# Optimization experiments

Measured on AMD Instinct MI355X. Metric: run time of the kernel, lower is better.

The kernel has to match this reference:

```python
import jax, jax.numpy as jnp
import numpy as np


def setup_inputs() -> dict:
    key = jax.random.key(0)
    ks = jax.random.split(key, 7)
    t, e, h = 2048, 512, 8
    s = 0.02
    return {
        "x": jax.random.normal(ks[0], (t, e), jnp.float32),
        "y": jax.random.normal(ks[1], (t, e), jnp.float32),
        "Wk": jax.random.normal(ks[2], (e, e * h), jnp.float32) * s,
        "Wq": jax.random.normal(ks[3], (e, e * h), jnp.float32) * s,
        "Wv": jax.random.normal(ks[4], (e, e * h), jnp.float32) * s,
        "Wu": jax.random.normal(ks[5], (e * h, e), jnp.float32) * s,
        "bu": jnp.zeros((e,), jnp.float32),
    }


def reference(x, y, Wk, Wq, Wv, Wu, bu):
    t, e = x.shape
    h = Wk.shape[1] // e
    scale = e ** (-0.25)
    # projections -> [h, t, e] (head dim equals emb in this 'wide' attention)
    k = (x @ Wk).reshape(t, h, e).transpose(1, 0, 2) * scale
    q = (y @ Wq).reshape(t, h, e).transpose(1, 0, 2) * scale
    v = (x @ Wv).reshape(t, h, e).transpose(1, 0, 2)
    # scores [h, t, t]
    dot = jnp.einsum('hte,hse->hts', q, k)
    attn = jax.nn.softmax(dot, axis=-1)
    out = jnp.einsum('hts,hse->hte', attn, v)          # [h, t, e]
    out = out.transpose(1, 0, 2).reshape(t, h * e)     # [t, h*e]
    return (out @ Wu + bu)[None]                       # [1, t, e] (b=1 in original)
```

## Files before the change

### kernel.cpp

```cpp
#include <hip/hip_runtime.h>
#include <hip/hip_bf16.h>
#include <stdint.h>

#define T_SEQ 2048
#define EMB   512
#define NH    8
#define HEAD_ALL 4096

typedef __attribute__((ext_vector_type(8))) short short8;
typedef __attribute__((ext_vector_type(4))) float f32x4;

__device__ __forceinline__ unsigned short f2b(float f) {
    __hip_bfloat16 h = __float2bfloat16(f);
    return *reinterpret_cast<unsigned short*>(&h);
}
__device__ __forceinline__ float b2f(unsigned short u) {
    return __uint_as_float(((unsigned)u) << 16);
}
__device__ __forceinline__ void gload_lds16(const void* g, void* l) {
    __builtin_amdgcn_global_load_lds((__attribute__((address_space(1))) void*)(void*)(g),
                                     (__attribute__((address_space(3))) void*)(l), 16, 0, 0);
}
__device__ __forceinline__ void wg_barrier() {
    asm volatile("" ::: "memory");
    __builtin_amdgcn_s_barrier();
    asm volatile("" ::: "memory");
}

__global__ void cvt_bf16_2(const float* __restrict__ a, const float* __restrict__ b,
                           unsigned short* __restrict__ oa, unsigned short* __restrict__ ob, int n8) {
    const float* in = blockIdx.y ? b : a;
    unsigned short* out = blockIdx.y ? ob : oa;
    int i = blockIdx.x * 256 + threadIdx.x;
    if (i >= n8) return;
    const f32x4* p = (const f32x4*)in + 2 * (size_t)i;
    f32x4 va = p[0], vb = p[1];
    uint4 o;
    o.x = (unsigned)f2b(va[0]) | ((unsigned)f2b(va[1]) << 16);
    o.y = (unsigned)f2b(va[2]) | ((unsigned)f2b(va[3]) << 16);
    o.z = (unsigned)f2b(vb[0]) | ((unsigned)f2b(vb[1]) << 16);
    o.w = (unsigned)f2b(vb[2]) | ((unsigned)f2b(vb[3]) << 16);
    *((uint4*)out + i) = o;
}

__global__ void transpose_cvt3_f32(const float* __restrict__ w0, const float* __restrict__ w1,
                                   const float* __restrict__ w2, unsigned short* __restrict__ out,
                                   int R, int C, long outS) {
    __shared__ unsigned short t[64][66];
    const int z = blockIdx.z;
    const float* in = (z == 0) ? w0 : ((z == 1) ? w1 : w2);
    unsigned short* ob = out + (long)z * outS;
    const int tid = threadIdx.x;
    const int r0 = blockIdx.y * 64, c0 = blockIdx.x * 64;
#pragma unroll
    for (int it = 0; it < 4; ++it) {
        int flat = it * 256 + tid;
        int r = flat >> 4, c4 = flat & 15;
        f32x4 v = *(const f32x4*)(in + (long)(r0 + r) * C + c0 + c4 * 4);
#pragma unroll
        for (int w = 0; w < 4; ++w) t[r][c4 * 4 + w] = f2b(v[w]);
    }
    __syncthreads();
#pragma unroll
    for (int it = 0; it < 2; ++it) {
        int flat = it * 256 + tid;
        int rr = flat >> 3, c8 = flat & 7;
        unsigned u[4];
#pragma unroll
        for (int w = 0; w < 4; ++w) {
            unsigned short a = t[c8 * 8 + 2 * w][rr];
            unsigned short b = t[c8 * 8 + 2 * w + 1][rr];
            u[w] = (unsigned)a | ((unsigned)b << 16);
        }
        *(uint4*)(ob + (long)(c0 + rr) * R + r0 + c8 * 8) = make_uint4(u[0], u[1], u[2], u[3]);
    }
}

__global__ void transpose_bf16(const unsigned short* __restrict__ in, unsigned short* __restrict__ out,
                               int R, int C, long inS, long outS) {
    __shared__ unsigned short t[64][66];
    const unsigned short* ib = in + (long)blockIdx.z * inS;
    unsigned short* ob = out + (long)blockIdx.z * outS;
    const int tid = threadIdx.x;
    const int r0 = blockIdx.y * 64, c0 = blockIdx.x * 64;
#pragma unroll
    for (int it = 0; it < 2; ++it) {
        int flat = it * 256 + tid;
        int r = flat >> 3, c8 = flat & 7;
        uint4 v = *(const uint4*)(ib + (long)(r0 + r) * C + c0 + c8 * 8);
        unsigned u[4] = {v.x, v.y, v.z, v.w};
#pragma unroll
        for (int w = 0; w < 4; ++w) {
            t[r][c8 * 8 + 2 * w]     = (unsigned short)(u[w] & 0xffff);
            t[r][c8 * 8 + 2 * w + 1] = (unsigned short)(u[w] >> 16);
        }
    }
    __syncthreads();
#pragma unroll
    for (int it = 0; it < 2; ++it) {
        int flat = it * 256 + tid;
        int rr = flat >> 3, c8 = flat & 7;
        unsigned u[4];
#pragma unroll
        for (int w = 0; w < 4; ++w)
            u[w] = (unsigned)t[c8 * 8 + 2 * w][rr] | ((unsigned)t[c8 * 8 + 2 * w + 1][rr] << 16);
        *(uint4*)(ob + (long)(c0 + rr) * R + r0 + c8 * 8) = make_uint4(u[0], u[1], u[2], u[3]);
    }
}

template<int R_>
__device__ __forceinline__ void stage2(const unsigned short* __restrict__ src, int kfull,
                                       short* ldsbase, int i, int tid, int wid) {
#pragma unroll
    for (int s = 0; s < 2; ++s) {
        const int ii = i + s;
        const int r = ii * 64 + (tid >> 3);
        const int d = (tid & 7) * 16;
        const int sc = (d ^ ((r & 7) << 4)) >> 1;
        gload_lds16(src + (long)r * kfull + sc, ldsbase + ii * 4096 + wid * 512);
    }
}

template<int BM, int BN, int KTILES, int MODE>
__global__ __launch_bounds__(512, 2)
void gemm8p(const unsigned short* __restrict__ A, const unsigned short* __restrict__ A2,
            const unsigned short* __restrict__ B, void* __restrict__ Cout,
            int kfull, float alpha, long As, long Bs, long Cs, int ldc)
{
    static_assert(KTILES >= 3, "pipeline needs >=3 K-tiles");
    constexpr int ATILE = BM * 64;
    constexpr int BTILE = BN * 64;
    constexpr int LA = BM / 64;
    constexpr int LB = BN / 64;
    constexpr int MF = BM / 32;
    constexpr int NF = BN / 64;
    constexpr int MFP = MF / 4;

    __shared__ __align__(16) short lds[2 * (ATILE + BTILE)];

    const int tid = threadIdx.x;
    const int wid = tid >> 6, lane = tid & 63;
    const int wm = wid >> 2, wn = wid & 3;
    const int fr = lane & 15, fq = lane >> 4;

    const int nwg = gridDim.x * gridDim.y * gridDim.z;
    int flat = blockIdx.x + gridDim.x * (blockIdx.y + gridDim.y * blockIdx.z);
    flat = (flat & 7) * (nwg >> 3) + (flat >> 3);
    const int bx = flat % gridDim.x;
    const int rem = flat / gridDim.x;
    const int by = rem % gridDim.y;
    const long batch = rem / gridDim.y;

    const int bm = by * BM, bn = bx * BN;

    const unsigned short* Ab;
    const unsigned short* Bb;
    int koff = 0;
    if constexpr (MODE == 1) { Ab = (batch == 2) ? A2 : A; Bb = B + batch * Bs; }
    else { Ab = A; Bb = B; koff = (int)batch * (KTILES * 64); }

    const unsigned short* Ag = Ab + (long)bm * kfull + koff;
    const unsigned short* Bg = Bb + (long)bn * kfull + koff;

    f32x4 acc[MF][NF];
#pragma unroll
    for (int i = 0; i < MF; i++)
#pragma unroll
        for (int j = 0; j < NF; j++) acc[i][j] = 0.f;

#pragma unroll
    for (int i = 0; i < LA; i += 2) stage2<BM>(Ag, kfull, lds, i, tid, wid);
#pragma unroll
    for (int i = 0; i < LB; i += 2) stage2<BN>(Bg, kfull, lds + 2 * ATILE, i, tid, wid);
#pragma unroll
    for (int i = 0; i < LB; i += 2) stage2<BN>(Bg + 64, kfull, lds + 2 * ATILE + BTILE, i, tid, wid);
    if constexpr (LB == 4) asm volatile("s_waitcnt vmcnt(4)" ::: "memory");
    else                   asm volatile("s_waitcnt vmcnt(2)" ::: "memory");
    wg_barrier();

#pragma unroll 2
    for (int t = 0; t < KTILES; ++t) {
        short* la  = lds + (t & 1) * ATILE;
        short* laN = lds + ((t + 1) & 1) * ATILE;
        short* lb  = lds + 2 * ATILE + (t & 1) * BTILE;
        const int kA = (t + 1) * 64;
        const int kB = (t + 2) * 64;

        short8 bfrag[NF][2];
#pragma unroll
        for (int q = 0; q < 4; ++q) {
            if (q == 0) {
#pragma unroll
                for (int nf = 0; nf < NF; ++nf)
#pragma unroll
                    for (int kk = 0; kk < 2; ++kk) {
                        const int r = wn * (BN / 4) + nf * 16 + fr;
                        const int cb = kk * 64 + fq * 16;
                        bfrag[nf][kk] = *(const short8*)(lb + r * 64 + ((cb ^ ((r & 7) << 4)) >> 1));
                    }
            }
            short8 afrag[MFP][2];
#pragma unroll
            for (int mf = 0; mf < MFP; ++mf)
#pragma unroll
                for (int kk = 0; kk < 2; ++kk) {
                    const int r = wm * (BM / 2) + q * (BM / 8) + mf * 16 + fr;
                    const int cb = kk * 64 + fq * 16;
                    afrag[mf][kk] = *(const short8*)(la + r * 64 + ((cb ^ ((r & 7) << 4)) >> 1));
                }
            if (t + 1 < KTILES) {
                if (q == 0) stage2<BM>(Ag + kA, kfull, laN, 0, tid, wid);
                if (q == 1 && LA == 4) stage2<BM>(Ag + kA, kfull, laN, 2, tid, wid);
            }
            if (t + 2 < KTILES) {
                if (q == 2) stage2<BN>(Bg + kB, kfull, lb, 0, tid, wid);
                if (q == 3 && LB == 4) stage2<BN>(Bg + kB, kfull, lb, 2, tid, wid);
            }
            wg_barrier();
            __builtin_amdgcn_s_setprio(1);
#pragma unroll
            for (int mf = 0; mf < MFP; ++mf)
#pragma unroll
                for (int nf = 0; nf < NF; ++nf)
#pragma unroll
                    for (int kk = 0; kk < 2; ++kk)
                        acc[q * MFP + mf][nf] = __builtin_amdgcn_mfma_f32_16x16x32_bf16(
                            afrag[mf][kk], bfrag[nf][kk], acc[q * MFP + mf][nf], 0, 0, 0);
            __builtin_amdgcn_s_setprio(0);
            if (q == 3) {
                if (t + 2 < KTILES) {
                    if constexpr (LB == 4) asm volatile("s_waitcnt vmcnt(4)" ::: "memory");
                    else                   asm volatile("s_waitcnt vmcnt(2)" ::: "memory");
                } else {
                    asm volatile("s_waitcnt vmcnt(0)" ::: "memory");
                }
            }
            wg_barrier();
        }
    }

#pragma unroll
    for (int m = 0; m < MF; ++m)
#pragma unroll
        for (int j = 0; j < 4; ++j) {
            const int row = bm + wm * (BM / 2) + m * 16 + fq * 4 + j;
#pragma unroll
            for (int n = 0; n < NF; ++n) {
                const int col = bn + wn * (BN / 4) + n * 16 + fr;
                const float v = acc[m][n][j] * alpha;
                if constexpr (MODE == 1) {
                    unsigned short* C = (unsigned short*)Cout + batch * Cs;
                    C[(long)(col >> 9) * ((long)T_SEQ * EMB) + (long)row * EMB + (col & 511)] = f2b(v);
                } else {
                    float* C = (float*)Cout + batch * ((long)T_SEQ * EMB);
                    C[(long)row * ldc + col] = v;
                }
            }
        }
}

__global__ __launch_bounds__(512, 1)
void attn_fused(const unsigned short* __restrict__ Qg, const unsigned short* __restrict__ Kg,
                const unsigned short* __restrict__ VTg, unsigned short* __restrict__ Og,
                float scale)
{
    __shared__ __align__(16) short lds[69888];
    float* rs = (float*)(lds + 69632);
    char* ldsb = (char*)lds;

    const int tid = threadIdx.x;
    const int wid = tid >> 6, lane = tid & 63;
    const int fr = lane & 15, fq = lane >> 4;
    const int rg = wid >> 1, ch = wid & 1;

    const int orig = blockIdx.x + 32 * blockIdx.y;
    const int f = (orig & 7) * 32 + (orig >> 3);
    const int qb = f & 31, h = f >> 5;
    const long TE = (long)T_SEQ * EMB;
    const unsigned short* Qh = Qg + (long)h * TE + (long)(qb * 64) * EMB;
    const unsigned short* Kh = Kg + (long)h * TE;
    const unsigned short* Vh = VTg + (long)h * TE;

    short8 qreg[16];
#pragma unroll
    for (int ks = 0; ks < 16; ++ks)
        qreg[ks] = *(const short8*)(Qh + (long)(rg * 16 + fr) * EMB + ks * 32 + fq * 8);

    auto stageK = [&](int kb) {
#pragma unroll
        for (int it = 0; it < 8; ++it) {
            const int c = it * 512 + tid;
            const int kv = c >> 6, s = c & 63;
            gload_lds16(Kh + (long)(kb * 64 + kv) * EMB + (((s * 16) ^ ((kv & 7) << 4)) >> 1),
                        lds + (it * 512 + wid * 64) * 8);
        }
    };
    auto stageV = [&](int kb) {
#pragma unroll
        for (int it = 0; it < 8; ++it) {
            const int c = it * 512 + tid;
            const int d = c >> 3, s = c & 7;
            gload_lds16(Vh + (long)d * T_SEQ + kb * 64 + (((s * 16) ^ ((d & 7) << 4)) >> 1),
                        lds + 32768 + (it * 512 + wid * 64) * 8);
        }
    };

    f32x4 oacc[4][4];
#pragma unroll
    for (int m = 0; m < 4; ++m)
#pragma unroll
        for (int n = 0; n < 4; ++n) oacc[m][n] = 0.f;
    float rsum[4] = {0.f, 0.f, 0.f, 0.f};

    stageK(0);
    stageV(0);

#pragma unroll 1
    for (int t = 0; t < 32; ++t) {
        asm volatile("s_waitcnt vmcnt(8)" ::: "memory");
        wg_barrier();

        f32x4 sacc[2][2];
#pragma unroll
        for (int c = 0; c < 2; ++c) { sacc[c][0] = 0.f; sacc[c][1] = 0.f; }
#pragma unroll
        for (int ks = 0; ks < 16; ++ks) {
#pragma unroll
            for (int c = 0; c < 2; ++c) {
                const int kv = (ch * 2 + c) * 16 + fr;
                const short8 bfr = *(const short8*)(ldsb + kv * 1024 +
                                    ((ks * 64 + fq * 16) ^ ((kv & 7) << 4)));
                sacc[c][ks & 1] = __builtin_amdgcn_mfma_f32_16x16x32_bf16(
                    qreg[ks], bfr, sacc[c][ks & 1], 0, 0, 0);
            }
        }
#pragma unroll
        for (int c = 0; c < 2; ++c)
#pragma unroll
            for (int j = 0; j < 4; ++j) {
                const float v = __expf(scale * (sacc[c][0][j] + sacc[c][1][j]));
                rsum[j] += v;
                const int row = rg * 16 + fq * 4 + j;
                const int kv = (ch * 2 + c) * 16 + fr;
                *(unsigned short*)(ldsb + 131072 + row * 128 +
                    ((kv * 2) ^ ((row & 7) << 4) ^ ((row & 8) << 2))) = f2b(v);
            }
        asm volatile("s_waitcnt lgkmcnt(0)" ::: "memory");
        asm volatile("s_waitcnt vmcnt(0)" ::: "memory");
        wg_barrier();
        if (t + 1 < 32) stageK(t + 1);

#pragma unroll
        for (int kk = 0; kk < 2; ++kk) {
            short8 sa[4], vb[4];
#pragma unroll
            for (int m = 0; m < 4; ++m) {
                const int row = m * 16 + fr;
                sa[m] = *(const short8*)(ldsb + 131072 + row * 128 +
                          ((kk * 64 + fq * 16) ^ ((row & 7) << 4) ^ ((row & 8) << 2)));
            }
#pragma unroll
            for (int n = 0; n < 4; ++n) {
                const int d = wid * 64 + n * 16 + fr;
                vb[n] = *(const short8*)(ldsb + 65536 + d * 128 +
                          ((kk * 64 + fq * 16) ^ ((d & 7) << 4)));
            }
            __builtin_amdgcn_s_setprio(1);
#pragma unroll
            for (int m = 0; m < 4; ++m)
#pragma unroll
                for (int n = 0; n < 4; ++n)
                    oacc[m][n] = __builtin_amdgcn_mfma_f32_16x16x32_bf16(
                        sa[m], vb[n], oacc[m][n], 0, 0, 0);
            __builtin_amdgcn_s_setprio(0);
        }
        wg_barrier();
        if (t + 1 < 32) stageV(t + 1);
    }

#pragma unroll
    for (int j = 0; j < 4; ++j) {
        float v = rsum[j];
        v += __shfl_xor(v, 1);
        v += __shfl_xor(v, 2);
        v += __shfl_xor(v, 4);
        v += __shfl_xor(v, 8);
        if (fr == 0) rs[ch * 64 + rg * 16 + fq * 4 + j] = v;
    }
    asm volatile("s_waitcnt lgkmcnt(0)" ::: "memory");
    wg_barrier();

#pragma unroll
    for (int m = 0; m < 4; ++m)
#pragma unroll
        for (int j = 0; j < 4; ++j) {
            const int row = m * 16 + fq * 4 + j;
            const float rinv = 1.0f / (rs[row] + rs[64 + row]);
#pragma unroll
            for (int n = 0; n < 4; ++n) {
                const int d = wid * 64 + n * 16 + fr;
                Og[(long)(qb * 64 + row) * HEAD_ALL + h * EMB + d] = f2b(oacc[m][n][j] * rinv);
            }
        }
}

__global__ void reduce_bias(const float* __restrict__ part, const float* __restrict__ bias,
                            float* __restrict__ out) {
    const int i = blockIdx.x * 256 + threadIdx.x;
    const long stride4 = (long)T_SEQ * EMB / 4;
    const f32x4* p = (const f32x4*)part;
    f32x4 s = p[i];
#pragma unroll
    for (int sl = 1; sl < 8; ++sl) s += p[i + sl * stride4];
    f32x4 b = *(const f32x4*)(bias + ((i * 4) % EMB));
    *((f32x4*)out + i) = s + b;
}

extern "C" void kernel_launch(void* const* d_in, const int* in_sizes, int n_in,
                              void* d_out, int out_size, void* d_ws, size_t ws_size,
                              hipStream_t stream)
{
    const float* x  = (const float*)d_in[0];
    const float* y  = (const float*)d_in[1];
    const float* Wk = (const float*)d_in[2];
    const float* Wq = (const float*)d_in[3];
    const float* Wv = (const float*)d_in[4];
    const float* Wu = (const float*)d_in[5];
    const float* bu = (const float*)d_in[6];
    char* ws = (char*)d_ws;
    const size_t MB = 1024ull * 1024ull;

    unsigned short* xb   = (unsigned short*)(ws + 0);
    unsigned short* yb   = (unsigned short*)(ws + 2 * MB);
    unsigned short* WT3  = (unsigned short*)(ws + 4 * MB);
    unsigned short* PRJ  = (unsigned short*)(ws + 48 * MB);
    unsigned short* Vb   = (unsigned short*)(ws + 48 * MB);
    unsigned short* Kb   = (unsigned short*)(ws + 64 * MB);
    unsigned short* Qb   = (unsigned short*)(ws + 80 * MB);
    unsigned short* WuT  = (unsigned short*)(ws + 96 * MB);
    unsigned short* VTb  = (unsigned short*)(ws + 100 * MB);
    unsigned short* Ob   = (unsigned short*)(ws + 116 * MB);
    float*          part = (float*)(ws + 0);

    const float scale2 = 0.04419417382415922f;
    const long TE = (long)T_SEQ * EMB;

    cvt_bf16_2<<<dim3(512, 2), dim3(256), 0, stream>>>(x, y, xb, yb, T_SEQ * EMB / 8);
    transpose_cvt3_f32<<<dim3(HEAD_ALL / 64, EMB / 64, 3), dim3(256), 0, stream>>>(
        Wv, Wk, Wq, WT3, EMB, HEAD_ALL, (long)2 * MB);
    transpose_cvt3_f32<<<dim3(EMB / 64, HEAD_ALL / 64, 1), dim3(256), 0, stream>>>(
        Wu, nullptr, nullptr, WuT, HEAD_ALL, EMB, 0);

    gemm8p<256, 256, 8, 1><<<dim3(HEAD_ALL / 256, T_SEQ / 256, 3), 512, 0, stream>>>(
        xb, yb, WT3, PRJ, EMB, 1.f, 0, (long)2 * MB, (long)8 * MB, 0);

    transpose_bf16<<<dim3(EMB / 64, T_SEQ / 64, NH), dim3(256), 0, stream>>>(
        Vb, VTb, T_SEQ, EMB, TE, TE);

    attn_fused<<<dim3(32, 8), 512, 0, stream>>>(Qb, Kb, VTb, Ob, scale2);

    gemm8p<256, 128, 8, 3><<<dim3(EMB / 128, T_SEQ / 256, 8), 512, 0, stream>>>(
        Ob, nullptr, WuT, part, HEAD_ALL, 1.f, 0, 0, 0, EMB);

    reduce_bias<<<dim3(T_SEQ * EMB / 4 / 256), dim3(256), 0, stream>>>(part, bu, (float*)d_out);
}
```

Before: 181.1 us.

## Software-pipeline attention: double-buffer 32-key K/V tiles and overlap QK with PV

Shrinks the key block from 64 to 32 and double-buffers the K, V and probability tiles in LDS. Each iteration computes QK^T for block t while running P·V for block t-1, with a drain step after the loop. The goal is to cut the per-iteration barrier and wait stalls between the score and output phases and let MFMA work overlap the global-to-LDS loads. In exchange the loop runs twice as many iterations, each with less work per barrier, and the LDS swizzle patterns change.

```diff
diff --git a/kernel.cpp b/kernel.cpp
--- a/kernel.cpp
+++ b/kernel.cpp
@@ -265,8 +265,8 @@
                 float scale)
 {
     __shared__ __align__(16) short lds[69888];
-    float* rs = (float*)(lds + 69632);
-    char* ldsb = (char*)lds;
+    char* L = (char*)lds;
+    float* rs = (float*)(L + 139264);
 
     const int tid = threadIdx.x;
     const int wid = tid >> 6, lane = tid & 63;
@@ -286,22 +286,22 @@
     for (int ks = 0; ks < 16; ++ks)
         qreg[ks] = *(const short8*)(Qh + (long)(rg * 16 + fr) * EMB + ks * 32 + fq * 8);
 
-    auto stageK = [&](int kb) {
-#pragma unroll
-        for (int it = 0; it < 8; ++it) {
+    auto stK = [&](int kb, int buf) {
+#pragma unroll
+        for (int it = 0; it < 4; ++it) {
             const int c = it * 512 + tid;
             const int kv = c >> 6, s = c & 63;
-            gload_lds16(Kh + (long)(kb * 64 + kv) * EMB + (((s * 16) ^ ((kv & 7) << 4)) >> 1),
-                        lds + (it * 512 + wid * 64) * 8);
+            gload_lds16(Kh + (long)(kb * 32 + kv) * EMB + (((s * 16) ^ ((kv & 7) << 4)) >> 1),
+                        L + buf + (it * 512 + wid * 64) * 16);
         }
     };
-    auto stageV = [&](int kb) {
-#pragma unroll
-        for (int it = 0; it < 8; ++it) {
+    auto stV = [&](int kb, int buf) {
+#pragma unroll
+        for (int it = 0; it < 4; ++it) {
             const int c = it * 512 + tid;
-            const int d = c >> 3, s = c & 7;
-            gload_lds16(Vh + (long)d * T_SEQ + kb * 64 + (((s * 16) ^ ((d & 7) << 4)) >> 1),
-                        lds + 32768 + (it * 512 + wid * 64) * 8);
+            const int d = c >> 2, s = c & 3;
+            gload_lds16(Vh + (long)d * T_SEQ + kb * 32 + (((s * 16) ^ ((d & 3) << 4)) >> 1),
+                        L + buf + (it * 512 + wid * 64) * 16);
         }
     };
 
@@ -312,58 +312,43 @@
         for (int n = 0; n < 4; ++n) oacc[m][n] = 0.f;
     float rsum[4] = {0.f, 0.f, 0.f, 0.f};
 
-    stageK(0);
-    stageV(0);
+    const int kv = ch * 16 + fr;
+    const int swA = ((fr >> 2) & 3) << 4;
+
+    stK(0, 0);
+    stV(0, 65536);
 
 #pragma unroll 1
-    for (int t = 0; t < 32; ++t) {
-        asm volatile("s_waitcnt vmcnt(8)" ::: "memory");
+    for (int t = 0; t < 64; ++t) {
+        asm volatile("s_waitcnt vmcnt(4) lgkmcnt(0)" ::: "memory");
         wg_barrier();
-
-        f32x4 sacc[2][2];
-#pragma unroll
-        for (int c = 0; c < 2; ++c) { sacc[c][0] = 0.f; sacc[c][1] = 0.f; }
+        if (t + 1 < 64) stK(t + 1, ((t + 1) & 1) ? 32768 : 0);
+
+        const char* Kb_ = L + ((t & 1) ? 32768 : 0);
+        const char* Sp_ = L + 131072 + ((t & 1) ? 4096 : 0);
+        const char* Sr_ = L + 131072 + (((t - 1) & 1) ? 4096 : 0);
+        const char* Vr_ = L + 65536 + (((t - 1) & 1) ? 32768 : 0);
+
+        f32x4 sacc0 = 0.f, sacc1 = 0.f;
 #pragma unroll
         for (int ks = 0; ks < 16; ++ks) {
-#pragma unroll
-            for (int c = 0; c < 2; ++c) {
-                const int kv = (ch * 2 + c) * 16 + fr;
-                const short8 bfr = *(const short8*)(ldsb + kv * 1024 +
-                                    ((ks * 64 + fq * 16) ^ ((kv & 7) << 4)));
-                sacc[c][ks & 1] = __builtin_amdgcn_mfma_f32_16x16x32_bf16(
-                    qreg[ks], bfr, sacc[c][ks & 1], 0, 0, 0);
-            }
-        }
-#pragma unroll
-        for (int c = 0; c < 2; ++c)
-#pragma unroll
-            for (int j = 0; j < 4; ++j) {
-                const float v = __expf(scale * (sacc[c][0][j] + sacc[c][1][j]));
-                rsum[j] += v;
-                const int row = rg * 16 + fq * 4 + j;
-                const int kv = (ch * 2 + c) * 16 + fr;
-                *(unsigned short*)(ldsb + 131072 + row * 128 +
-                    ((kv * 2) ^ ((row & 7) << 4) ^ ((row & 8) << 2))) = f2b(v);
-            }
-        asm volatile("s_waitcnt lgkmcnt(0)" ::: "memory");
-        asm volatile("s_waitcnt vmcnt(0)" ::: "memory");
-        wg_barrier();
-        if (t + 1 < 32) stageK(t + 1);
-
-#pragma unroll
-        for (int kk = 0; kk < 2; ++kk) {
+            const short8 bfr = *(const short8*)(Kb_ + kv * 1024 +
+                                ((ks * 64 + fq * 16) ^ ((kv & 7) << 4)));
+            if (ks & 1) sacc1 = __builtin_amdgcn_mfma_f32_16x16x32_bf16(qreg[ks], bfr, sacc1, 0, 0, 0);
+            else        sacc0 = __builtin_amdgcn_mfma_f32_16x16x32_bf16(qreg[ks], bfr, sacc0, 0, 0, 0);
+        }
+
+        if (t > 0) {
             short8 sa[4], vb[4];
 #pragma unroll
             for (int m = 0; m < 4; ++m) {
                 const int row = m * 16 + fr;
-                sa[m] = *(const short8*)(ldsb + 131072 + row * 128 +
-                          ((kk * 64 + fq * 16) ^ ((row & 7) << 4) ^ ((row & 8) << 2)));
+                sa[m] = *(const short8*)(Sr_ + row * 64 + ((fq * 16) ^ swA));
             }
 #pragma unroll
             for (int n = 0; n < 4; ++n) {
                 const int d = wid * 64 + n * 16 + fr;
-                vb[n] = *(const short8*)(ldsb + 65536 + d * 128 +
-                          ((kk * 64 + fq * 16) ^ ((d & 7) << 4)));
+                vb[n] = *(const short8*)(Vr_ + d * 64 + ((fq * 16) ^ ((d & 3) << 4)));
             }
             __builtin_amdgcn_s_setprio(1);
 #pragma unroll
@@ -374,8 +359,42 @@
                         sa[m], vb[n], oacc[m][n], 0, 0, 0);
             __builtin_amdgcn_s_setprio(0);
         }
+
+#pragma unroll
+        for (int j = 0; j < 4; ++j) {
+            const float v = __expf(scale * (sacc0[j] + sacc1[j]));
+            rsum[j] += v;
+            const int row = rg * 16 + fq * 4 + j;
+            *(unsigned short*)((char*)Sp_ + row * 64 +
+                ((kv * 2) ^ (((row >> 2) & 3) << 4))) = f2b(v);
+        }
+
         wg_barrier();
-        if (t + 1 < 32) stageV(t + 1);
+        if (t + 1 < 64) stV(t + 1, 65536 + (((t + 1) & 1) ? 32768 : 0));
+    }
+
+    asm volatile("s_waitcnt vmcnt(0) lgkmcnt(0)" ::: "memory");
+    wg_barrier();
+    {
+        const char* Sr_ = L + 131072 + 4096;
+        const char* Vr_ = L + 65536 + 32768;
+        short8 sa[4], vb[4];
+#pragma unroll
+        for (int m = 0; m < 4; ++m) {
+            const int row = m * 16 + fr;
+            sa[m] = *(const short8*)(Sr_ + row * 64 + ((fq * 16) ^ swA));
+        }
+#pragma unroll
+        for (int n = 0; n < 4; ++n) {
+            const int d = wid * 64 + n * 16 + fr;
+            vb[n] = *(const short8*)(Vr_ + d * 64 + ((fq * 16) ^ ((d & 3) << 4)));
+        }
+#pragma unroll
+        for (int m = 0; m < 4; ++m)
+#pragma unroll
+            for (int n = 0; n < 4; ++n)
+                oacc[m][n] = __builtin_amdgcn_mfma_f32_16x16x32_bf16(
+                    sa[m], vb[n], oacc[m][n], 0, 0, 0);
     }
 
 #pragma unroll
```

Result: slower. 198.0 us (+9.3%).
